# Kernel tuning notes

Measured on AMD Instinct MI355X. Metric: run time of the kernel, lower is better.

## Reference

```python
import jax, jax.numpy as jnp
import numpy as np

B, T, IN_DIM = 256, 256, 64
HID, DIM2, OUT_DIM, N_HEADS = 1024, 512, 16, 32


def _linear(x, w, b):
    return x @ w.T + b


def _gru(x, h0, w_ih, w_hh, b_ih, b_hh):
    # x: [B,T,HID], h0: [B,HID]; returns final hidden [B,HID]
    gi_all = jnp.einsum('bti,gi->btg', x, w_ih) + b_ih  # [B,T,3H] precomputed input gates
    def step(h, gi):
        gh = h @ w_hh.T + b_hh
        i_r, i_z, i_n = jnp.split(gi, 3, axis=-1)
        h_r, h_z, h_n = jnp.split(gh, 3, axis=-1)
        r = jax.nn.sigmoid(i_r + h_r)
        z = jax.nn.sigmoid(i_z + h_z)
        n = jnp.tanh(i_n + r * h_n)
        h_new = (1.0 - z) * n + z * h
        return h_new, None
    h, _ = jax.lax.scan(step, h0, jnp.swapaxes(gi_all, 0, 1))
    return h


def setup_inputs() -> dict:
    key = jax.random.key(0)
    ks = jax.random.split(key, 16)
    s = 0.05
    inp = {
        'input': jax.random.normal(ks[0], (B, T, IN_DIM), jnp.float32),
        'hn': jnp.zeros((1, B, HID), jnp.float32),
        'cultivars': jax.random.randint(ks[1], (B, 1), 0, N_HEADS, jnp.int32),
        'fc1_w': jax.random.normal(ks[2], (DIM2, IN_DIM), jnp.float32) * s,
        'fc1_b': jnp.zeros((DIM2,), jnp.float32),
        'fc2_w': jax.random.normal(ks[3], (HID, DIM2), jnp.float32) * s,
        'fc2_b': jnp.zeros((HID,), jnp.float32),
        'w_ih': jax.random.normal(ks[4], (3 * HID, HID), jnp.float32) * s,
        'w_hh': jax.random.normal(ks[5], (3 * HID, HID), jnp.float32) * s,
        'b_ih': jnp.zeros((3 * HID,), jnp.float32),
        'b_hh': jnp.zeros((3 * HID,), jnp.float32),
        'fc3_w': jax.random.normal(ks[6], (DIM2, HID), jnp.float32) * s,
        'fc3_b': jnp.zeros((DIM2,), jnp.float32),
        'heads_w': jax.random.normal(ks[7], (N_HEADS, OUT_DIM, DIM2), jnp.float32) * s,
        'heads_b': jnp.zeros((N_HEADS, OUT_DIM), jnp.float32),
    }
    return inp


def reference(input, hn, cultivars, fc1_w, fc1_b, fc2_w, fc2_b, w_ih, w_hh, b_ih, b_hh, fc3_w, fc3_b, heads_w, heads_b):
    x = _linear(input, fc1_w, fc1_b)          # [B,T,DIM2]
    x = _linear(x, fc2_w, fc2_b)              # [B,T,HID]
    h = _gru(x, hn[0], w_ih, w_hh, b_ih, b_hh)  # [B,HID]
    hn_out = h[None]                          # [1,B,HID]
    out = jax.nn.relu(hn_out)
    out = jax.nn.relu(_linear(out, fc3_w, fc3_b))[0]  # [B,DIM2]
    cidx = cultivars[:, 0]                    # [B]
    w_sel = heads_w[cidx]                     # [B,OUT_DIM,DIM2] gathered head weights
    b_sel = heads_b[cidx]                     # [B,OUT_DIM]
    params = jnp.einsum('bd,bod->bo', out, w_sel) + b_sel
    return params, hn_out
```

## Files before the change

kernel.cpp:

```cpp
#include <hip/hip_runtime.h>

#define T_   256
#define HID_ 1024
#define D2   512

typedef __attribute__((ext_vector_type(8))) short  short8;
typedef __attribute__((ext_vector_type(8))) __bf16 bf16x8;
typedef __attribute__((ext_vector_type(4))) float  f32x4;

__device__ __forceinline__ float sigmoidf_(float x) {
    return __fdividef(1.0f, 1.0f + __expf(-x));
}
__device__ __forceinline__ float tanhf_(float x) {
    return 1.0f - __fdividef(2.0f, 1.0f + __expf(2.0f * x));
}
__device__ __forceinline__ unsigned short bf16hi(float x) {
    unsigned u = __float_as_uint(x);
    return (unsigned short)((u + 0x7FFFu + ((u >> 16) & 1u)) >> 16);
}
__device__ __forceinline__ float bf2f(unsigned short h) {
    return __uint_as_float((unsigned)h << 16);
}
__device__ __forceinline__ f32x4 mfma_(short8 a, short8 b, f32x4 c) {
    union { short8 s; bf16x8 b; } ua, ub;
    ua.s = a; ub.s = b;
    return __builtin_amdgcn_mfma_f32_16x16x32_bf16(ua.b, ub.b, c, 0, 0, 0);
}

__device__ __forceinline__ void gl16(short8& d, const void* p) {
    asm volatile("global_load_dwordx4 %0, %1, off" : "=v"(d) : "v"(p));
}
__device__ __forceinline__ void gl16c(short8& d, const void* p) {
    asm volatile("global_load_dwordx4 %0, %1, off sc0 sc1" : "=v"(d) : "v"(p));
}
__device__ __forceinline__ void gs8c(void* p, unsigned long long v) {
    asm volatile("global_store_dwordx2 %0, %1, off sc0 sc1"
                 :: "v"(p), "v"(v) : "memory");
}
#define WAITV0() asm volatile("s_waitcnt vmcnt(0)" ::: "memory")
#define WAITV8() asm volatile("s_waitcnt vmcnt(8)" ::: "memory")
#define WAITV10_TIE(H, L) asm volatile("s_waitcnt vmcnt(10)" : "+v"(H), "+v"(L) :: "memory")
#define WAITV2_TIE(H, L)  asm volatile("s_waitcnt vmcnt(2)"  : "+v"(H), "+v"(L) :: "memory")
#define WAITV0_TIE(H, L)  asm volatile("s_waitcnt vmcnt(0)"  : "+v"(H), "+v"(L) :: "memory")
#define ABAR() asm volatile("s_waitcnt lgkmcnt(0)\n\ts_barrier" ::: "memory")

__global__ __launch_bounds__(256) void k_w2(
    const float* __restrict__ fc2_w, const float* __restrict__ fc1_w,
    const float* __restrict__ fc1_b, const float* __restrict__ fc2_b,
    float* __restrict__ W2, float* __restrict__ b2)
{
    int idx = blockIdx.x * 256 + threadIdx.x;
    int r = idx >> 6, c = idx & 63;
    float acc = 0.f;
    for (int k = 0; k < D2; ++k)
        acc += fc2_w[(size_t)r * D2 + k] * fc1_w[(size_t)k * 64 + c];
    W2[idx] = acc;
    if (c == 0) {
        float a = fc2_b[r];
        for (int k = 0; k < D2; ++k)
            a += fc2_w[(size_t)r * D2 + k] * fc1_b[k];
        b2[r] = a;
    }
}

__global__ __launch_bounds__(256) void k_wc(
    const float* __restrict__ w_ih, const float* __restrict__ W2,
    const float* __restrict__ b2, const float* __restrict__ b_ih,
    unsigned short* __restrict__ wc_hi, unsigned short* __restrict__ wc_lo,
    float* __restrict__ bc)
{
    int idx = blockIdx.x * 256 + threadIdx.x;
    int r = idx >> 6, c = idx & 63;
    float acc = 0.f;
    for (int k = 0; k < HID_; ++k)
        acc += w_ih[(size_t)r * HID_ + k] * W2[(size_t)k * 64 + c];
    unsigned short h = bf16hi(acc);
    wc_hi[idx] = h;
    wc_lo[idx] = bf16hi(acc - bf2f(h));
    if (c == 0) {
        float a = b_ih[r];
        for (int k = 0; k < HID_; ++k)
            a += w_ih[(size_t)r * HID_ + k] * b2[k];
        bc[r] = a;
    }
}

__global__ __launch_bounds__(256) void k_splitw(
    const float* __restrict__ w, unsigned short* __restrict__ hi,
    unsigned short* __restrict__ lo)
{
    int i4 = (blockIdx.x * 256 + threadIdx.x) * 4;
    float4 v = *(const float4*)(w + i4);
    float vv[4] = {v.x, v.y, v.z, v.w};
    unsigned short h4[4], l4[4];
    #pragma unroll
    for (int i = 0; i < 4; ++i) {
        h4[i] = bf16hi(vv[i]);
        l4[i] = bf16hi(vv[i] - bf2f(h4[i]));
    }
    *(unsigned long long*)(hi + i4) =
        (unsigned long long)h4[0] | ((unsigned long long)h4[1] << 16) |
        ((unsigned long long)h4[2] << 32) | ((unsigned long long)h4[3] << 48);
    *(unsigned long long*)(lo + i4) =
        (unsigned long long)l4[0] | ((unsigned long long)l4[1] << 16) |
        ((unsigned long long)l4[2] << 32) | ((unsigned long long)l4[3] << 48);
}

__global__ __launch_bounds__(256) void k_split_h0(
    const float* __restrict__ hn, unsigned short* __restrict__ hi,
    unsigned short* __restrict__ lo)
{
    int gid = blockIdx.x * 256 + threadIdx.x;
    int b = gid >> 7, kseg = gid & 127;
    const float* src = hn + (size_t)b * HID_ + kseg * 8;
    short8 h8, l8;
    #pragma unroll
    for (int i = 0; i < 8; ++i) {
        float v = src[i];
        unsigned short h = bf16hi(v);
        ((short*)&h8)[i] = (short)h;
        ((short*)&l8)[i] = (short)bf16hi(v - bf2f(h));
    }
    size_t off = (size_t)(kseg >> 2) * 8192 + b * 32 + (kseg & 3) * 8;
    *(short8*)(hi + off) = h8;
    *(short8*)(lo + off) = l8;
}

__global__ __launch_bounds__(256, 1) void k_gru(
    const float* __restrict__ input,
    const float* __restrict__ hn,
    const float* __restrict__ b_hh,
    const float* __restrict__ bc,
    const unsigned short* __restrict__ whh_hi,
    const unsigned short* __restrict__ whh_lo,
    const unsigned short* __restrict__ wc_hi,
    const unsigned short* __restrict__ wc_lo,
    unsigned short* __restrict__ hxA_hi, unsigned short* __restrict__ hxA_lo,
    unsigned short* __restrict__ hxB_hi, unsigned short* __restrict__ hxB_lo,
    float* __restrict__ hn_out,
    int* __restrict__ bar)
{
    const int g = blockIdx.x, ct = g & 31, bt = g >> 5;
    const int j0 = ct << 5, b0 = bt << 5;
    const int tid = threadIdx.x, lane = tid & 63, wid = tid >> 6;
    const int mh = wid & 1, kh = wid >> 1;
    const int l15 = lane & 15, quad = lane >> 4;

    __shared__ short smB[36864];
    float* smF = (float*)smB;
    const int SIN_ = 4672, SHN_ = 6784;

    const int t7 = tid & 127, pl = tid >> 7;
    const unsigned short* wsrc = pl ? whh_lo : whh_hi;
    const unsigned short* csrc = pl ? wc_lo : wc_hi;
    const char* wB[3]; const char* cB[3]; int lo_[3];
    #pragma unroll
    for (int i = 0; i < 3; ++i) {
        int sid = t7 + (i << 7);
        int n = sid >> 2, ss = sid & 3;
        int grow = (n >> 5) * HID_ + j0 + (n & 31);
        wB[i] = (const char*)wsrc + (size_t)grow * 2048u + (size_t)ss * 16u;
        cB[i] = (const char*)csrc + (size_t)grow * 128u + (size_t)ss * 16u;
        lo_[i] = (pl * 96 + n) * 32 + ((ss * 8) ^ (((n >> 1) & 3) << 3));
    }
    const int foff = l15 * 32 + ((quad * 8) ^ (((l15 >> 1) & 3) << 3));
    const size_t aoff = (size_t)((b0 + mh * 16 + l15) * 64 + quad * 16);
    const char* aAh = (const char*)hxA_hi + aoff;
    const char* aAl = (const char*)hxA_lo + aoff;
    const char* aBh = (const char*)hxB_hi + aoff;
    const char* aBl = (const char*)hxB_lo + aoff;
    const float* xrow = input + (size_t)(b0 + mh * 16 + l15) * (T_ * 64)
                              + kh * 32 + quad * 8;

    const int gb = tid >> 3, gj4 = (tid & 7) << 2;
    float hreg[4], br[4], bz[4], bni[4], bnh[4];
    #pragma unroll
    for (int i = 0; i < 4; ++i) {
        int j = j0 + gj4 + i;
        hreg[i] = hn[(size_t)(b0 + gb) * HID_ + j];
        br[i]  = bc[j] + b_hh[j];
        bz[i]  = bc[1024 + j] + b_hh[1024 + j];
        bni[i] = bc[2048 + j];
        bnh[i] = b_hh[2048 + j];
    }
    const size_t hoff = (size_t)(ct * 16384 + (b0 + gb) * 64 + gj4 * 2);
    char* sAh = (char*)hxA_hi + hoff; char* sAl = (char*)hxA_lo + hoff;
    char* sBh = (char*)hxB_hi + hoff; char* sBl = (char*)hxB_lo + hoff;
    const int g73 = gb * 73, g33 = gb * 33;

    int* arrive  = bar + bt * 128;
    int* release = bar + bt * 128 + 32;

    short8 bp[2][6];
    short8 ab[3][2];
    f32x4 acc[6], acci[2];

#define GH_CHUNK(RB, AH, AL)                                                  \
  { _Pragma("unroll")                                                         \
    for (int nt = 0; nt < 6; ++nt) {                                          \
        short8 bh_ = *(const short8*)(smB + (RB) + nt * 512 + foff);          \
        short8 bl_ = *(const short8*)(smB + (RB) + 3072 + nt * 512 + foff);   \
        f32x4 v_ = mfma_(AH, bh_, acc[nt]);                                   \
        v_ = mfma_(AH, bl_, v_);                                              \
        v_ = mfma_(AL, bh_, v_);                                              \
        acc[nt] = v_; } }

    #pragma unroll 1
    for (int t = 0; t < 256; ++t) {
        const char* rh = (t & 1) ? aBh : aAh;
        const char* rl = (t & 1) ? aBl : aAl;
        char* wh = (t & 1) ? sAh : sBh;
        char* wl = (t & 1) ? sAl : sBl;

        short8 gp[6];
        #pragma unroll
        for (int j = 0; j < 6; ++j)
            gl16(gp[j], cB[j % 3] + (j / 3) * 64);
        float xv[8];
        *(float4*)&xv[0] = *(const float4*)(xrow + (size_t)t * 64);
        *(float4*)&xv[4] = *(const float4*)(xrow + (size_t)t * 64 + 4);
        short8 xa_hi, xa_lo;
        #pragma unroll
        for (int i = 0; i < 8; ++i) {
            unsigned short h = bf16hi(xv[i]);
            ((short*)&xa_hi)[i] = (short)h;
            ((short*)&xa_lo)[i] = (short)bf16hi(xv[i] - bf2f(h));
        }
        WAITV0();
        #pragma unroll
        for (int j = 0; j < 6; ++j)
            *(short8*)(smB + (j / 3) * 6144 + lo_[j % 3]) = gp[j];
        #pragma unroll
        for (int j = 0; j < 6; ++j)
            gl16(bp[0][j], wB[j % 3] + (size_t)(j / 3) * 64);
        #pragma unroll
        for (int j = 0; j < 6; ++j)
            gl16(bp[1][j], wB[j % 3] + (size_t)(2 + j / 3) * 64);
        ABAR();
        {
            const int rb = kh * 6144;
            #pragma unroll
            for (int nt = 0; nt < 6; ++nt) {
                short8 bh_ = *(const short8*)(smB + rb + nt * 512 + foff);
                short8 bl_ = *(const short8*)(smB + rb + 3072 + nt * 512 + foff);
                f32x4 z = {0.f, 0.f, 0.f, 0.f};
                f32x4 v = mfma_(xa_hi, bh_, z);
                v = mfma_(xa_hi, bl_, v);
                v = mfma_(xa_lo, bh_, v);
                if (nt < 4) { acc[nt] = v; }
                else { acci[nt - 4] = v; acc[nt] = z; }
            }
        }
        if (t > 0 && tid == 0) {
            while (__hip_atomic_load(release, __ATOMIC_RELAXED,
                                     __HIP_MEMORY_SCOPE_SYSTEM) < t)
                __builtin_amdgcn_s_sleep(4);
        }
        ABAR();
        gl16c(ab[0][0], rh + (size_t)kh * 16384);
        gl16c(ab[0][1], rl + (size_t)kh * 16384);
        WAITV8();
        #pragma unroll
        for (int j = 0; j < 6; ++j)
            *(short8*)(smB + (j / 3) * 6144 + lo_[j % 3]) = bp[0][j];
        gl16c(ab[1][0], rh + (size_t)(2 + kh) * 16384);
        gl16c(ab[1][1], rl + (size_t)(2 + kh) * 16384);
        ABAR();
        #pragma unroll
        for (int G = 0; G < 16; ++G) {
            if (G <= 13) {
                #pragma unroll
                for (int j = 0; j < 6; ++j)
                    gl16(bp[G & 1][j],
                         wB[j % 3] + (size_t)(2 * G + 4 + j / 3) * 64);
                gl16c(ab[(G + 2) % 3][0], rh + (size_t)(2 * (G + 2) + kh) * 16384);
                gl16c(ab[(G + 2) % 3][1], rl + (size_t)(2 * (G + 2) + kh) * 16384);
                WAITV10_TIE(ab[G % 3][0], ab[G % 3][1]);
            } else if (G == 14) {
                WAITV2_TIE(ab[2][0], ab[2][1]);
            } else {
                WAITV0_TIE(ab[0][0], ab[0][1]);
            }
            if (G <= 14) {
                #pragma unroll
                for (int j = 0; j < 6; ++j)
                    *(short8*)(smB + ((G + 1) % 3) * 12288 + (j / 3) * 6144
                               + lo_[j % 3]) = bp[(G + 1) & 1][j];
                ABAR();
            }
            GH_CHUNK((G % 3) * 12288 + kh * 6144, ab[G % 3][0], ab[G % 3][1]);
        }
        __syncthreads();
        {
            const int row = mh * 16 + quad * 4;
            #pragma unroll
            for (int nt = 0; nt < 4; ++nt)
                #pragma unroll
                for (int r = 0; r < 4; ++r)
                    smF[kh * 2336 + (row + r) * 73 + nt * 16 + l15] = acc[nt][r];
            #pragma unroll
            for (int jn = 0; jn < 2; ++jn)
                #pragma unroll
                for (int r = 0; r < 4; ++r) {
                    smF[SHN_ + kh * 1056 + (row + r) * 33 + jn * 16 + l15] = acc[4 + jn][r];
                    smF[SIN_ + kh * 1056 + (row + r) * 33 + jn * 16 + l15] = acci[jn][r];
                }
        }
        __syncthreads();
        unsigned short ph4[4], pl4[4];
        #pragma unroll
        for (int i = 0; i < 4; ++i) {
            int cl = gj4 + i;
            float rp = smF[g73 + cl] + smF[2336 + g73 + cl] + br[i];
            float zp = smF[g73 + 32 + cl] + smF[2336 + g73 + 32 + cl] + bz[i];
            float ip = smF[SIN_ + g33 + cl] + smF[SIN_ + 1056 + g33 + cl] + bni[i];
            float hp = smF[SHN_ + g33 + cl] + smF[SHN_ + 1056 + g33 + cl] + bnh[i];
            float rr = sigmoidf_(rp);
            float zz = sigmoidf_(zp);
            float nn = tanhf_(ip + rr * hp);
            float hv = (1.0f - zz) * nn + zz * hreg[i];
            hreg[i] = hv;
            unsigned short hh = bf16hi(hv);
            ph4[i] = hh;
            pl4[i] = bf16hi(hv - bf2f(hh));
        }
        unsigned long long pk_hi =
            (unsigned long long)ph4[0] | ((unsigned long long)ph4[1] << 16) |
            ((unsigned long long)ph4[2] << 32) | ((unsigned long long)ph4[3] << 48);
        unsigned long long pk_lo =
            (unsigned long long)pl4[0] | ((unsigned long long)pl4[1] << 16) |
            ((unsigned long long)pl4[2] << 32) | ((unsigned long long)pl4[3] << 48);
        gs8c(wh, pk_hi);
        gs8c(wl, pk_lo);
        if (t == 255) {
            #pragma unroll
            for (int i = 0; i < 4; ++i)
                hn_out[(size_t)(b0 + gb) * HID_ + j0 + gj4 + i] = hreg[i];
        }
        WAITV0();
        __syncthreads();
        if (t < 255 && tid == 0) {
            int old = __hip_atomic_fetch_add(arrive, 1, __ATOMIC_RELAXED,
                                             __HIP_MEMORY_SCOPE_SYSTEM);
            if (old == ((t + 1) << 5) - 1)
                __hip_atomic_store(release, t + 1, __ATOMIC_RELAXED,
                                   __HIP_MEMORY_SCOPE_SYSTEM);
        }
    }
#undef GH_CHUNK
}

__global__ __launch_bounds__(256) void k_fc3(
    const float* __restrict__ h, const float* __restrict__ fc3_w,
    const float* __restrict__ fc3_b, float* __restrict__ out3)
{
    const int bt = blockIdx.x >> 3;
    const int dt = blockIdx.x & 7;
    const int b0 = bt << 6;
    const int d0 = dt << 6;
    const int tid = threadIdx.x;
    const int tx = tid & 15, ty = tid >> 4;

    __shared__ float sh_h[64][36];
    __shared__ float sh_w[64][36];

    float acc[4][4] = {};
    const int lr = tid >> 3;
    const int lc = (tid & 7) << 2;

    for (int kk = 0; kk < HID_; kk += 32) {
        #pragma unroll
        for (int p = 0; p < 2; ++p) {
            int row = lr + (p << 5);
            float4 v = *(const float4*)(h + (size_t)(b0 + row) * HID_ + kk + lc);
            v.x = fmaxf(v.x, 0.f); v.y = fmaxf(v.y, 0.f);
            v.z = fmaxf(v.z, 0.f); v.w = fmaxf(v.w, 0.f);
            *(float4*)&sh_h[row][lc] = v;
            *(float4*)&sh_w[row][lc] =
                *(const float4*)(fc3_w + (size_t)(d0 + row) * HID_ + kk + lc);
        }
        __syncthreads();
        #pragma unroll
        for (int k = 0; k < 32; ++k) {
            float hv[4], wv[4];
            #pragma unroll
            for (int i = 0; i < 4; ++i) hv[i] = sh_h[ty + (i << 4)][k];
            #pragma unroll
            for (int q = 0; q < 4; ++q) wv[q] = sh_w[tx + (q << 4)][k];
            #pragma unroll
            for (int i = 0; i < 4; ++i)
                #pragma unroll
                for (int q = 0; q < 4; ++q)
                    acc[i][q] += hv[i] * wv[q];
        }
        __syncthreads();
    }
    #pragma unroll
    for (int i = 0; i < 4; ++i) {
        int b = b0 + ty + (i << 4);
        #pragma unroll
        for (int q = 0; q < 4; ++q) {
            int d = d0 + tx + (q << 4);
            out3[(size_t)b * D2 + d] = fmaxf(acc[i][q] + fc3_b[d], 0.f);
        }
    }
}

__global__ __launch_bounds__(256) void k_heads(
    const float* __restrict__ out3, const int* __restrict__ cult,
    const float* __restrict__ hw, const float* __restrict__ hb,
    float* __restrict__ params)
{
    int b = blockIdx.x;
    int o = threadIdx.x >> 4;
    int l = threadIdx.x & 15;
    int cid = cult[b];
    const float* w = hw + ((size_t)cid * 16 + o) * D2;
    const float* x = out3 + (size_t)b * D2;
    float acc = 0.f;
    #pragma unroll
    for (int m = 0; m < 8; ++m) {
        int d4 = (l + (m << 4)) << 2;
        float4 xv = *(const float4*)(x + d4);
        float4 wv = *(const float4*)(w + d4);
        acc += xv.x * wv.x + xv.y * wv.y + xv.z * wv.z + xv.w * wv.w;
    }
    #pragma unroll
    for (int s = 1; s < 16; s <<= 1)
        acc += __shfl_xor(acc, s, 16);
    if (l == 0)
        params[(size_t)b * 16 + o] = acc + hb[(size_t)cid * 16 + o];
}

extern "C" void kernel_launch(void* const* d_in, const int* in_sizes, int n_in,
                              void* d_out, int out_size, void* d_ws, size_t ws_size,
                              hipStream_t stream)
{
    const float* input = (const float*)d_in[0];
    const float* hn    = (const float*)d_in[1];
    const int*   cult  = (const int*)d_in[2];
    const float* fc1_w = (const float*)d_in[3];
    const float* fc1_b = (const float*)d_in[4];
    const float* fc2_w = (const float*)d_in[5];
    const float* fc2_b = (const float*)d_in[6];
    const float* w_ih  = (const float*)d_in[7];
    const float* w_hh  = (const float*)d_in[8];
    const float* b_ih  = (const float*)d_in[9];
    const float* b_hh  = (const float*)d_in[10];
    const float* fc3_w = (const float*)d_in[11];
    const float* fc3_b = (const float*)d_in[12];
    const float* hw    = (const float*)d_in[13];
    const float* hb    = (const float*)d_in[14];
    float* out = (float*)d_out;
    float* hn_out = out + 4096;

    char* ws = (char*)d_ws;
    int*   bar    = (int*)ws;
    float* W2     = (float*)(ws + 4096);
    float* b2     = (float*)(ws + 266240);
    float* bc     = (float*)(ws + 270336);
    unsigned short* whh_hi = (unsigned short*)(ws + 282624);
    unsigned short* whh_lo = (unsigned short*)(ws + 282624 + 6291456);
    unsigned short* wc_hi  = (unsigned short*)(ws + 12865536);
    unsigned short* wc_lo  = (unsigned short*)(ws + 13258752);
    unsigned short* hxA_hi = (unsigned short*)(ws + 13651968);
    unsigned short* hxA_lo = (unsigned short*)(ws + 14176256);
    unsigned short* hxB_hi = (unsigned short*)(ws + 14700544);
    unsigned short* hxB_lo = (unsigned short*)(ws + 15224832);
    float* out3   = (float*)(ws + 15749120);

    hipMemsetAsync(bar, 0, 4096, stream);
    k_w2<<<256, 256, 0, stream>>>(fc2_w, fc1_w, fc1_b, fc2_b, W2, b2);
    k_wc<<<768, 256, 0, stream>>>(w_ih, W2, b2, b_ih, wc_hi, wc_lo, bc);
    k_splitw<<<3072, 256, 0, stream>>>(w_hh, whh_hi, whh_lo);
    k_split_h0<<<128, 256, 0, stream>>>(hn, hxA_hi, hxA_lo);
    k_gru<<<256, 256, 0, stream>>>(input, hn, b_hh, bc,
                                   whh_hi, whh_lo, wc_hi, wc_lo,
                                   hxA_hi, hxA_lo, hxB_hi, hxB_lo,
                                   hn_out, bar);
    k_fc3<<<32, 256, 0, stream>>>(hn_out, fc3_w, fc3_b, out3);
    k_heads<<<256, 256, 0, stream>>>(out3, cult, hw, hb, out);
}
```

Measured before the change: 3.137 ms.

## Double per-stage K chunk in GRU recurrence pipeline to halve barriers

Restructures the per-timestep W_hh streaming pipeline so that each stage covers four 64-wide K chunks instead of two. That gives 8 stages instead of 16, with a triple-buffered LDS ring twice as large, and the hidden-state (A) loads are double-buffered in groups of four. The aim is to halve the number of LDS barriers and wait points per timestep and to keep more loads in flight. In exchange, LDS use doubles to 144KB and register pressure rises from the 12-register weight prefetch buffer, which may reduce latency hiding or cause spills.

```diff
diff --git a/kernel.cpp b/kernel.cpp
--- a/kernel.cpp
+++ b/kernel.cpp
@@ -38,10 +38,11 @@
                  :: "v"(p), "v"(v) : "memory");
 }
 #define WAITV0() asm volatile("s_waitcnt vmcnt(0)" ::: "memory")
-#define WAITV8() asm volatile("s_waitcnt vmcnt(8)" ::: "memory")
-#define WAITV10_TIE(H, L) asm volatile("s_waitcnt vmcnt(10)" : "+v"(H), "+v"(L) :: "memory")
-#define WAITV2_TIE(H, L)  asm volatile("s_waitcnt vmcnt(2)"  : "+v"(H), "+v"(L) :: "memory")
-#define WAITV0_TIE(H, L)  asm volatile("s_waitcnt vmcnt(0)"  : "+v"(H), "+v"(L) :: "memory")
+#define WAITV4() asm volatile("s_waitcnt vmcnt(4)" ::: "memory")
+#define WAITV4_TIE4(A0, A1, A2, A3) asm volatile("s_waitcnt vmcnt(4)" \
+    : "+v"(A0), "+v"(A1), "+v"(A2), "+v"(A3) :: "memory")
+#define WAITV0_TIE4(A0, A1, A2, A3) asm volatile("s_waitcnt vmcnt(0)" \
+    : "+v"(A0), "+v"(A1), "+v"(A2), "+v"(A3) :: "memory")
 #define ABAR() asm volatile("s_waitcnt lgkmcnt(0)\n\ts_barrier" ::: "memory")
 
 __global__ __launch_bounds__(256) void k_w2(
@@ -146,7 +147,7 @@
     const int mh = wid & 1, kh = wid >> 1;
     const int l15 = lane & 15, quad = lane >> 4;
 
-    __shared__ short smB[36864];
+    __shared__ short smB[73728];
     float* smF = (float*)smB;
     const int SIN_ = 4672, SHN_ = 6784;
 
@@ -191,10 +192,28 @@
     int* arrive  = bar + bt * 128;
     int* release = bar + bt * 128 + 32;
 
-    short8 bp[2][6];
-    short8 ab[3][2];
+    short8 bp[12];
+    short8 ab[2][2][2];
     f32x4 acc[6], acci[2];
 
+#define ISSUE_W(GG)                                                           \
+  { _Pragma("unroll")                                                         \
+    for (int cc_ = 0; cc_ < 4; ++cc_)                                         \
+        _Pragma("unroll")                                                     \
+        for (int i_ = 0; i_ < 3; ++i_)                                        \
+            gl16(bp[cc_ * 3 + i_], wB[i_] + (size_t)(4 * (GG) + cc_) * 64); }
+#define WRITE_W(GG)                                                           \
+  { _Pragma("unroll")                                                         \
+    for (int cc_ = 0; cc_ < 4; ++cc_)                                         \
+        _Pragma("unroll")                                                     \
+        for (int i_ = 0; i_ < 3; ++i_)                                        \
+            *(short8*)(smB + ((GG) % 3) * 24576 + cc_ * 6144 + lo_[i_]) =     \
+                bp[cc_ * 3 + i_]; }
+#define ISSUE_A(BK, GG)                                                       \
+  { gl16c(ab[BK][0][0], rh + (size_t)(4 * (GG) + kh) * 16384);                \
+    gl16c(ab[BK][0][1], rl + (size_t)(4 * (GG) + kh) * 16384);                \
+    gl16c(ab[BK][1][0], rh + (size_t)(4 * (GG) + 2 + kh) * 16384);            \
+    gl16c(ab[BK][1][1], rl + (size_t)(4 * (GG) + 2 + kh) * 16384); }
 #define GH_CHUNK(RB, AH, AL)                                                  \
   { _Pragma("unroll")                                                         \
     for (int nt = 0; nt < 6; ++nt) {                                          \
@@ -230,12 +249,7 @@
         #pragma unroll
         for (int j = 0; j < 6; ++j)
             *(short8*)(smB + (j / 3) * 6144 + lo_[j % 3]) = gp[j];
-        #pragma unroll
-        for (int j = 0; j < 6; ++j)
-            gl16(bp[0][j], wB[j % 3] + (size_t)(j / 3) * 64);
-        #pragma unroll
-        for (int j = 0; j < 6; ++j)
-            gl16(bp[1][j], wB[j % 3] + (size_t)(2 + j / 3) * 64);
+        ISSUE_W(0);
         ABAR();
         {
             const int rb = kh * 6144;
@@ -257,38 +271,29 @@
                 __builtin_amdgcn_s_sleep(4);
         }
         ABAR();
-        gl16c(ab[0][0], rh + (size_t)kh * 16384);
-        gl16c(ab[0][1], rl + (size_t)kh * 16384);
-        WAITV8();
-        #pragma unroll
-        for (int j = 0; j < 6; ++j)
-            *(short8*)(smB + (j / 3) * 6144 + lo_[j % 3]) = bp[0][j];
-        gl16c(ab[1][0], rh + (size_t)(2 + kh) * 16384);
-        gl16c(ab[1][1], rl + (size_t)(2 + kh) * 16384);
+        ISSUE_A(0, 0);
+        WAITV4();
+        WRITE_W(0);
+        ISSUE_W(1);
+        ISSUE_A(1, 1);
         ABAR();
         #pragma unroll
-        for (int G = 0; G < 16; ++G) {
-            if (G <= 13) {
-                #pragma unroll
-                for (int j = 0; j < 6; ++j)
-                    gl16(bp[G & 1][j],
-                         wB[j % 3] + (size_t)(2 * G + 4 + j / 3) * 64);
-                gl16c(ab[(G + 2) % 3][0], rh + (size_t)(2 * (G + 2) + kh) * 16384);
-                gl16c(ab[(G + 2) % 3][1], rl + (size_t)(2 * (G + 2) + kh) * 16384);
-                WAITV10_TIE(ab[G % 3][0], ab[G % 3][1]);
-            } else if (G == 14) {
-                WAITV2_TIE(ab[2][0], ab[2][1]);
+        for (int G = 0; G < 8; ++G) {
+            if (G <= 6) {
+                WAITV4_TIE4(ab[G & 1][0][0], ab[G & 1][0][1],
+                            ab[G & 1][1][0], ab[G & 1][1][1]);
+                WRITE_W(G + 1);
+                if (G <= 5) ISSUE_W(G + 2);
+                ABAR();
             } else {
-                WAITV0_TIE(ab[0][0], ab[0][1]);
+                WAITV0_TIE4(ab[1][0][0], ab[1][0][1],
+                            ab[1][1][0], ab[1][1][1]);
             }
-            if (G <= 14) {
-                #pragma unroll
-                for (int j = 0; j < 6; ++j)
-                    *(short8*)(smB + ((G + 1) % 3) * 12288 + (j / 3) * 6144
-                               + lo_[j % 3]) = bp[(G + 1) & 1][j];
-                ABAR();
-            }
-            GH_CHUNK((G % 3) * 12288 + kh * 6144, ab[G % 3][0], ab[G % 3][1]);
+            GH_CHUNK((G % 3) * 24576 + kh * 6144,
+                     ab[G & 1][0][0], ab[G & 1][0][1]);
+            GH_CHUNK((G % 3) * 24576 + (2 + kh) * 6144,
+                     ab[G & 1][1][0], ab[G & 1][1][1]);
+            if (G <= 5) ISSUE_A(G & 1, G + 2);
         }
         __syncthreads();
         {
@@ -348,6 +353,9 @@
         }
     }
 #undef GH_CHUNK
+#undef ISSUE_A
+#undef WRITE_W
+#undef ISSUE_W
 }
 
 __global__ __launch_bounds__(256) void k_fc3(
```

Measured after the change: 3.278 ms. 4.5% more time.
